# Kernel optimization log

Hardware: AMD Instinct MI355X
Metric: run time of the kernel (lower is better)

Reference implementation:

```python
import jax, jax.numpy as jnp
import numpy as np

PIANO_SAMPLES = 2_621_440          # multiple of 256 (~119 s @ 22050 Hz)
BLOCK = 512
HOP = 256
N_STEPS = PIANO_SAMPLES // HOP      # 10240 loop iterations
N_FRAMES = PIANO_SAMPLES // HOP + 2 # 10242
UPSAMPLE = 256 // 32                # 8, as in F.upsample(scale_factor=8)


def _hamming(n=BLOCK):
    # torch.hamming_window default: periodic=True
    return (0.54 - 0.46 * jnp.cos(2.0 * jnp.pi * jnp.arange(n, dtype=jnp.float32) / n)).astype(jnp.float32)


def _upsample_linear(v, scale):
    # F.upsample(mode='linear', align_corners=False) on a 1D signal
    n = v.shape[0]
    coords = (jnp.arange(n * scale, dtype=jnp.float32) + 0.5) / scale - 0.5
    coords = jnp.clip(coords, 0.0, n - 1.0)
    lo = jnp.floor(coords).astype(jnp.int32)
    hi = jnp.minimum(lo + 1, n - 1)
    w = coords - lo.astype(jnp.float32)
    return v[lo] * (1.0 - w) + v[hi] * w


def setup_inputs() -> dict:
    key = jax.random.key(0)
    k1, k2, k3, k4, k5, k6 = jax.random.split(key, 6)
    return {
        "x": jnp.zeros((1,), jnp.float32),  # unused by the original forward
        "excitation_env": jax.random.uniform(k1, (N_FRAMES * 32,), jnp.float32) * 0.01,
        "tf_real": jax.random.uniform(k2, (N_FRAMES, 257), jnp.float32) * 0.2,
        "tf_imag": jax.random.uniform(k3, (N_FRAMES, 257), jnp.float32) * 0.2,
        "etf_real": jax.random.uniform(k4, (257,), jnp.float32) * 0.2,
        "etf_imag": jax.random.uniform(k5, (257,), jnp.float32) * 0.2,
        # per-step uniform(-1,1) noise (torch draws this inside forward)
        "noise": jax.random.uniform(k6, (N_STEPS, BLOCK), jnp.float32) * 2.0 - 1.0,
    }


def reference(x, excitation_env, tf_real, tf_imag, etf_real, etf_imag, noise):
    tf = (tf_real + 1j * tf_imag).astype(jnp.complex64)      # [N_FRAMES, 257]
    etf = (etf_real + 1j * etf_imag).astype(jnp.complex64)   # [257]
    win = _hamming()

    # excitation envelope: square then linear-upsample x8 -> len PIANO_SAMPLES + 512
    exc = _upsample_linear(excitation_env ** 2, UPSAMPLE)

    # gather all 512-sample excitation windows at hop 256 -> [N_STEPS, 512]
    idx = jnp.arange(N_STEPS)[:, None] * HOP + jnp.arange(BLOCK)[None, :]
    exc_blocks = exc[idx]

    # batched excitation filtering (independent per step -> fully vectorized)
    imp = noise * exc_blocks
    imp = jnp.fft.irfft(jnp.fft.rfft(imp, norm='ortho') * etf, norm='ortho').astype(jnp.float32)

    # impulse added to the *previous* block at steps 1..N_STEPS-1; last block gets none
    imp_next = jnp.concatenate([imp[1:], jnp.zeros((1, BLOCK), imp.dtype)], axis=0)

    def step(s, inp):
        tf_i, inext = inp
        b = win * jnp.fft.irfft(jnp.fft.rfft(s, norm='ortho') * tf_i, norm='ortho').astype(jnp.float32)
        s_next = b + inext
        return s_next, s_next

    s0 = imp[0]  # learned_impulse=False -> first block is the filtered excitation
    _, ys = jax.lax.scan(step, s0, (tf[:N_STEPS], imp_next))

    blocks = jnp.concatenate([s0[None, :], ys], axis=0)  # [N_STEPS+1, 512]

    # overlap-add with hop 256
    n_b = blocks.shape[0]
    out = jnp.zeros((n_b * HOP + (BLOCK - HOP),), blocks.dtype)
    oa_idx = jnp.arange(n_b)[:, None] * HOP + jnp.arange(BLOCK)[None, :]
    out = out.at[oa_idx].add(blocks)
    return out[:PIANO_SAMPLES]
```

## Files before the change

kernel.cpp:

```cpp
#include <hip/hip_runtime.h>
#include <math.h>

#define N_STEPS 10240
#define ROWF2 264
#define ROWF  (ROWF2*2)
#define ENV_N 327744
#define LCH 16

typedef float f4a __attribute__((ext_vector_type(4), aligned(4)));

__device__ inline float2 mkf2(float x, float y) { return make_float2(x, y); }

template<int DIR>
__device__ inline void waveFFT256(float2 v[4], const int l,
                                  const float Tc, const float Ts,
                                  const float ux, const float uy) {
  const int rb = (int)(__brev((unsigned)l) >> 26);
  #pragma unroll
  for (int r = 0; r < 4; ++r) {
    v[r].x = __shfl(v[r].x, rb);
    v[r].y = __shfl(v[r].y, rb);
  }
  #pragma unroll
  for (int s = 0; s < 6; ++s) {
    const int half = 1 << s;
    float wx, wy;
    if (s == 0) { wx = (l & 1) ? -1.f : 1.f; wy = 0.f; }
    else {
      const int idx = (l << (5 - s)) & 63;
      wx = __shfl(Tc, idx);
      float tsv = __shfl(Ts, idx);
      wy = (DIR < 0) ? tsv : -tsv;
    }
    #pragma unroll
    for (int r = 0; r < 4; ++r) {
      float tx = __shfl_xor(v[r].x, half);
      float ty = __shfl_xor(v[r].y, half);
      const bool low = (l & half) == 0;
      float ax = low ? v[r].x : tx, ay = low ? v[r].y : ty;
      float bx = low ? tx : v[r].x, by = low ? ty : v[r].y;
      v[r].x = ax + (wx * bx - wy * by);
      v[r].y = ay + (wx * by + wy * bx);
    }
  }
  const float u2x = ux * ux - uy * uy, u2y = 2.f * ux * uy;
  const float u3x = u2x * ux - u2y * uy, u3y = u2x * uy + u2y * ux;
  float2 t0 = v[0];
  float2 t1 = mkf2(v[1].x * ux - v[1].y * uy, v[1].x * uy + v[1].y * ux);
  float2 t2 = mkf2(v[2].x * u2x - v[2].y * u2y, v[2].x * u2y + v[2].y * u2x);
  float2 t3 = mkf2(v[3].x * u3x - v[3].y * u3y, v[3].x * u3y + v[3].y * u3x);
  float2 p02 = mkf2(t0.x + t2.x, t0.y + t2.y), m02 = mkf2(t0.x - t2.x, t0.y - t2.y);
  float2 p13 = mkf2(t1.x + t3.x, t1.y + t3.y), m13 = mkf2(t1.x - t3.x, t1.y - t3.y);
  v[0] = mkf2(p02.x + p13.x, p02.y + p13.y);
  v[2] = mkf2(p02.x - p13.x, p02.y - p13.y);
  if (DIR < 0) {
    v[1] = mkf2(m02.x + m13.y, m02.y - m13.x);
    v[3] = mkf2(m02.x - m13.y, m02.y + m13.x);
  } else {
    v[1] = mkf2(m02.x - m13.y, m02.y + m13.x);
    v[3] = mkf2(m02.x + m13.y, m02.y - m13.x);
  }
}

__global__ __launch_bounds__(256) void kernA(const float* __restrict__ env,
                                             const float* __restrict__ noise,
                                             const float* __restrict__ tf_re,
                                             const float* __restrict__ etf_re,
                                             const float* __restrict__ etf_im,
                                             float* __restrict__ IMP,
                                             float* __restrict__ T256,
                                             float* __restrict__ I256) {
  const int l = threadIdx.x & 63;
  const int j = blockIdx.x * 4 + (threadIdx.x >> 6);
  float* rowf = IMP + (size_t)j * ROWF;
  float2* row = (float2*)rowf;
  if (j >= N_STEPS) {
    if (j == N_STEPS) {
      #pragma unroll
      for (int r = 0; r < 4; ++r) row[64 * r + l] = mkf2(0.f, 0.f);
      if (l == 0) { row[256] = mkf2(0.f, 0.f); I256[N_STEPS] = 0.f; }
    }
    return;
  }
  const int K = 32 * j + l;
  float e0 = env[K];                e0 *= e0;
  float em = env[max(K - 1, 0)];    em *= em;
  float ep = env[min(K + 1, ENV_N - 1)]; ep *= ep;
  float sm[8];
  #pragma unroll
  for (int u = 0; u < 8; ++u) {
    float val;
    if (u < 4) {
      float fr = 0.5625f + 0.125f * (float)u;
      val = em * (1.f - fr) + e0 * fr;
      if (K == 0) val = e0;
    } else {
      float fr = 0.0625f + 0.125f * (float)(u - 4);
      val = e0 * (1.f - fr) + ep * fr;
    }
    sm[u] = val;
  }
  const float4* np = (const float4*)(noise + (size_t)j * 512 + 8 * l);
  float4 n0 = np[0], n1 = np[1];
  float nn[8] = {n0.x, n0.y, n0.z, n0.w, n1.x, n1.y, n1.z, n1.w};
  float2 v[4];
  #pragma unroll
  for (int r = 0; r < 4; ++r)
    v[r] = mkf2(nn[2 * r] * sm[2 * r], nn[2 * r + 1] * sm[2 * r + 1]);

  float ca, sa; sincosf(-0.01227184630308513f * (float)l, &sa, &ca);
  const float ux = ca * ca - sa * sa, uy = 2.f * ca * sa;
  float Tc, Ts; sincosf(-0.09817477042468103f * (float)l, &Ts, &Tc);

  waveFFT256<-1>(v, l, Tc, Ts, ux, uy);

  float2 Zc[4];
  const int pidx = (64 - l) & 63;
  #pragma unroll
  for (int r = 0; r < 4; ++r) {
    Zc[r].x = __shfl(v[3 - r].x, pidx);
    Zc[r].y = __shfl(v[3 - r].y, pidx);
  }
  float2 z0lane = v[0];
  if (l == 0) { Zc[0] = v[0]; Zc[1] = v[3]; Zc[2] = v[2]; Zc[3] = v[1]; }
  constexpr float crA[4] = {1.f, 0.7071067811865476f, 0.f, -0.7071067811865476f};
  constexpr float srA[4] = {0.f, -0.7071067811865476f, -1.f, -0.7071067811865476f};
  const float FS = 0.04419417382415922f;
  #pragma unroll
  for (int r = 0; r < 4; ++r) {
    float Ex = 0.5f * (v[r].x + Zc[r].x), Ey = 0.5f * (v[r].y - Zc[r].y);
    float Dx = v[r].x - Zc[r].x,          Dy = v[r].y + Zc[r].y;
    float Ox = 0.5f * Dy, Oy = -0.5f * Dx;
    float c  = crA[r] * ca - srA[r] * sa;
    float sn = crA[r] * sa + srA[r] * ca;
    float Wx = (Ex + (c * Ox - sn * Oy)) * FS;
    float Wy = (Ey + (c * Oy + sn * Ox)) * FS;
    int k = 64 * r + l;
    float er = etf_re[k], ei = etf_im[k];
    float Px = Wx * er - Wy * ei;
    float Py = Wx * ei + Wy * er;
    if (k == 0) Py = 0.f;
    row[k] = mkf2(Px, Py);
  }
  if (l == 0) {
    float W256 = (z0lane.x - z0lane.y) * FS;
    float imp256 = W256 * etf_re[256];
    row[256] = mkf2(imp256, 0.f);
    I256[j] = imp256;
    T256[j] = tf_re[(size_t)j * 257 + 256];
  }
}

struct StepBuf { f4a tr, ti; float4 ia, ib; };

__device__ inline void loadStep(StepBuf& b, int i, int l,
                                const float* __restrict__ tf_re,
                                const float* __restrict__ tf_im,
                                const float* __restrict__ IMP) {
  const size_t tb = (size_t)i * 257 + 4 * l;
  b.tr = *(const f4a*)(tf_re + tb);
  b.ti = *(const f4a*)(tf_im + tb);
  const float4* r4 = (const float4*)(IMP + (size_t)(i + 1) * ROWF);
  b.ia = r4[2 * l];
  b.ib = r4[2 * l + 1];
}

__device__ inline void doStep(const StepBuf& b, int l, float tfr256, float imp256,
                              float2& s0, float2& s1, float2& s2, float2& s3,
                              float& s256) {
  float2 y0, y1, y2, y3;
  y0.x = s0.x * b.tr[0] - s0.y * b.ti[0];  y0.y = s0.x * b.ti[0] + s0.y * b.tr[0];
  y1.x = s1.x * b.tr[1] - s1.y * b.ti[1];  y1.y = s1.x * b.ti[1] + s1.y * b.tr[1];
  y2.x = s2.x * b.tr[2] - s2.y * b.ti[2];  y2.y = s2.x * b.ti[2] + s2.y * b.tr[2];
  y3.x = s3.x * b.tr[3] - s3.y * b.ti[3];  y3.y = s3.x * b.ti[3] + s3.y * b.tr[3];
  if (l == 0) y0.y = 0.f;
  float Y256 = tfr256 * s256;
  float phx = __shfl_up(y3.x, 1), phy = __shfl_up(y3.y, 1);
  float nlx = __shfl_down(y0.x, 1), nly = __shfl_down(y0.y, 1);
  float2 p0 = (l == 0)  ? mkf2(y1.x, -y1.y) : mkf2(phx, phy);
  float2 n3 = (l == 63) ? mkf2(Y256, 0.f)   : mkf2(nlx, nly);
  float y255x = __shfl(y3.x, 63);
  const float A = 0.54f, Bc = 0.23f;
  float2 c0, c1, c2, c3;
  c0.x = A * y0.x - Bc * (p0.x + y1.x);  c0.y = A * y0.y - Bc * (p0.y + y1.y);
  c1.x = A * y1.x - Bc * (y0.x + y2.x);  c1.y = A * y1.y - Bc * (y0.y + y2.y);
  c2.x = A * y2.x - Bc * (y1.x + y3.x);  c2.y = A * y2.y - Bc * (y1.y + y3.y);
  c3.x = A * y3.x - Bc * (y2.x + n3.x);  c3.y = A * y3.y - Bc * (y2.y + n3.y);
  float C256 = A * Y256 - 0.46f * y255x;
  s0.x = c0.x + b.ia.x;  s0.y = c0.y + b.ia.y;
  s1.x = c1.x + b.ia.z;  s1.y = c1.y + b.ia.w;
  s2.x = c2.x + b.ib.x;  s2.y = c2.y + b.ib.y;
  s3.x = c3.x + b.ib.z;  s3.y = c3.y + b.ib.w;
  s256 = C256 + imp256;
}

__global__ __launch_bounds__(256, 2) void kernBC(const float* __restrict__ tf_re,
                                                 const float* __restrict__ tf_im,
                                                 const float* __restrict__ IMP,
                                                 const float* __restrict__ T256,
                                                 const float* __restrict__ I256,
                                                 float* __restrict__ out) {
  const int c = blockIdx.x, tid = threadIdx.x;
  const int l = tid & 63, w = tid >> 6;
  const int j0 = c * LCH;
  const int w0 = (c > 0) ? (j0 - 9) : 0;
  const int lastStep = (c > 0) ? (j0 + 14) : 15;

  __shared__ float2 ybuf[17][256];

  float t256v = T256[min(w0 + l, N_STEPS - 1)];
  float i256v = I256[min(w0 + 1 + l, N_STEPS)];

  float2 s0 = mkf2(0.f, 0.f), s1 = s0, s2 = s0, s3 = s0;
  float s256 = 0.f;
  float2 rs[5][4];
  float rn[5];
  #pragma unroll
  for (int q = 0; q < 5; ++q) {
    rs[q][0] = rs[q][1] = rs[q][2] = rs[q][3] = mkf2(0.f, 0.f);
    rn[q] = 0.f;
  }

  if (c == 0) {
    const float4* r4 = (const float4*)IMP;
    float4 a = r4[2 * l], bb = r4[2 * l + 1];
    s0 = mkf2(a.x, a.y);  s1 = mkf2(a.z, a.w);
    s2 = mkf2(bb.x, bb.y); s3 = mkf2(bb.z, bb.w);
    s256 = IMP[512];
    if (w == 1) { rs[0][0]=s0; rs[0][1]=s1; rs[0][2]=s2; rs[0][3]=s3; rn[0]=s256; }
  }

  StepBuf b0, b1, b2, b3;
  loadStep(b0, w0 + 0, l, tf_re, tf_im, IMP);
  loadStep(b1, w0 + 1, l, tf_re, tf_im, IMP);
  loadStep(b2, w0 + 2, l, tf_re, tf_im, IMP);
  loadStep(b3, w0 + 3, l, tf_re, tf_im, IMP);

  #define SAVEIF(KK) \
    if ((KK) >= 0 && (KK) <= 16 && (((KK) & 3) == w)) { \
      const int _q = (((KK) > 0 ? (KK) : 0)) >> 2; \
      rs[_q][0]=s0; rs[_q][1]=s1; rs[_q][2]=s2; rs[_q][3]=s3; rn[_q]=s256; }

  #define STEP(BUF, M, KK) { \
    const float tfr_ = __shfl(t256v, (M)); \
    const float im2_ = __shfl(i256v, (M)); \
    doStep(BUF, l, tfr_, im2_, s0, s1, s2, s3, s256); \
    SAVEIF(KK) \
    { int nx = w0 + (M) + 4; nx = (nx > lastStep) ? lastStep : nx; \
      loadStep(BUF, nx, l, tf_re, tf_im, IMP); } }

  if (c > 0) {
    STEP(b0,0,-7)  STEP(b1,1,-6)  STEP(b2,2,-5)  STEP(b3,3,-4)
    STEP(b0,4,-3)  STEP(b1,5,-2)  STEP(b2,6,-1)  STEP(b3,7,0)
    STEP(b0,8,1)   STEP(b1,9,2)   STEP(b2,10,3)  STEP(b3,11,4)
    STEP(b0,12,5)  STEP(b1,13,6)  STEP(b2,14,7)  STEP(b3,15,8)
    STEP(b0,16,9)  STEP(b1,17,10) STEP(b2,18,11) STEP(b3,19,12)
    STEP(b0,20,13) STEP(b1,21,14) STEP(b2,22,15) STEP(b3,23,16)
  } else {
    STEP(b0,0,2)   STEP(b1,1,3)   STEP(b2,2,4)   STEP(b3,3,5)
    STEP(b0,4,6)   STEP(b1,5,7)   STEP(b2,6,8)   STEP(b3,7,9)
    STEP(b0,8,10)  STEP(b1,9,11)  STEP(b2,10,12) STEP(b3,11,13)
    STEP(b0,12,14) STEP(b1,13,15) STEP(b2,14,16) STEP(b3,15,17)
  }
  #undef STEP
  #undef SAVEIF

  float cu, su; sincosf(0.02454369260617026f * (float)l, &su, &cu);
  const float clC = cu * cu - su * su, slC = 2.f * cu * su;
  float Tc, Ts; sincosf(-0.09817477042468103f * (float)l, &Ts, &Tc);
  constexpr float crC[4] = {1.f, 0.9999247018391445f, 0.9996988186962042f, 0.9993223845883495f};
  constexpr float srC[4] = {0.f, 0.0122715382857199f, 0.0245412285229123f, 0.0368072229413588f};
  const float ISC = 0.08838834764831845f;
  const int pidx = (64 - l) & 63;

  #pragma unroll
  for (int q = 0; q < 5; ++q) {
    const int k = 4 * q + w;
    if (k <= 16) {
      float2 W0 = rs[q][0], W1 = rs[q][1], W2 = rs[q][2], W3 = rs[q][3];
      float w256 = rn[q];
      float2 W[4] = {W0, W1, W2, W3};
      float2 Wm[4];
      Wm[0].x = __shfl(W0.x, pidx);
      Wm[0].y = __shfl(W0.y, pidx);
      if (l == 0) Wm[0] = mkf2(w256, 0.f);
      Wm[1].x = __shfl_xor(W3.x, 63);  Wm[1].y = __shfl_xor(W3.y, 63);
      Wm[2].x = __shfl_xor(W2.x, 63);  Wm[2].y = __shfl_xor(W2.y, 63);
      Wm[3].x = __shfl_xor(W1.x, 63);  Wm[3].y = __shfl_xor(W1.y, 63);
      float2 v[4];
      #pragma unroll
      for (int rr = 0; rr < 4; ++rr) {
        float Ex = 0.5f * (W[rr].x + Wm[rr].x), Ey = 0.5f * (W[rr].y - Wm[rr].y);
        float Dx = W[rr].x - Wm[rr].x,          Dy = W[rr].y + Wm[rr].y;
        float cc  = clC * crC[rr] - slC * srC[rr];
        float sn  = clC * srC[rr] + slC * crC[rr];
        float Ox = 0.5f * (cc * Dx - sn * Dy);
        float Oy = 0.5f * (cc * Dy + sn * Dx);
        v[rr] = mkf2(Ex - Oy, Ey + Ox);
      }
      waveFFT256<+1>(v, l, Tc, Ts, cu, su);
      #pragma unroll
      for (int rr = 0; rr < 4; ++rr)
        ybuf[k][64 * rr + l] = mkf2(v[rr].x * ISC, v[rr].y * ISC);
    }
  }

  __syncthreads();

  float2* out2 = (float2*)out;
  const size_t base = (size_t)j0 * 128;
  for (int idx = tid; idx < 2048; idx += 256) {
    const int k = idx >> 7, t2 = idx & 127;
    float2 a = ybuf[k + 1][t2];
    float2 p = ybuf[k][128 + t2];
    out2[base + idx] = mkf2(a.x + p.x, a.y + p.y);
  }
}

extern "C" void kernel_launch(void* const* d_in, const int* in_sizes, int n_in,
                              void* d_out, int out_size, void* d_ws, size_t ws_size,
                              hipStream_t stream) {
  const float* env    = (const float*)d_in[1];
  const float* tf_re  = (const float*)d_in[2];
  const float* tf_im  = (const float*)d_in[3];
  const float* etf_re = (const float*)d_in[4];
  const float* etf_im = (const float*)d_in[5];
  const float* noise  = (const float*)d_in[6];
  float* out = (float*)d_out;

  float* wsf = (float*)d_ws;
  float* IMP  = wsf;
  float* T256 = wsf + (size_t)(N_STEPS + 1) * ROWF;
  float* I256 = T256 + N_STEPS;

  kernA<<<(N_STEPS / 4) + 1, 256, 0, stream>>>(env, noise, tf_re, etf_re, etf_im,
                                               IMP, T256, I256);
  kernBC<<<N_STEPS / LCH, 256, 0, stream>>>(tf_re, tf_im, IMP, T256, I256, out);
}
```

Before: 49.73 us.

## Fuse excitation filtering into recurrence kernel via shared-memory impulse rows

```diff
diff --git a/kernel.cpp b/kernel.cpp
--- a/kernel.cpp
+++ b/kernel.cpp
@@ -2,8 +2,6 @@
 #include <math.h>
 
 #define N_STEPS 10240
-#define ROWF2 264
-#define ROWF  (ROWF2*2)
 #define ENV_N 327744
 #define LCH 16
 
@@ -62,26 +60,13 @@
   }
 }
 
-__global__ __launch_bounds__(256) void kernA(const float* __restrict__ env,
-                                             const float* __restrict__ noise,
-                                             const float* __restrict__ tf_re,
-                                             const float* __restrict__ etf_re,
-                                             const float* __restrict__ etf_im,
-                                             float* __restrict__ IMP,
-                                             float* __restrict__ T256,
-                                             float* __restrict__ I256) {
-  const int l = threadIdx.x & 63;
-  const int j = blockIdx.x * 4 + (threadIdx.x >> 6);
-  float* rowf = IMP + (size_t)j * ROWF;
-  float2* row = (float2*)rowf;
-  if (j >= N_STEPS) {
-    if (j == N_STEPS) {
-      #pragma unroll
-      for (int r = 0; r < 4; ++r) row[64 * r + l] = mkf2(0.f, 0.f);
-      if (l == 0) { row[256] = mkf2(0.f, 0.f); I256[N_STEPS] = 0.f; }
-    }
-    return;
-  }
+__device__ inline void impRow(int j, int l, float2* __restrict__ row,
+                              const float* __restrict__ env,
+                              const float* __restrict__ noise,
+                              const float* __restrict__ etf_re,
+                              const float* __restrict__ etf_im,
+                              float ca, float sa, float ux, float uy,
+                              float Tc, float Ts) {
   const int K = 32 * j + l;
   float e0 = env[K];                e0 *= e0;
   float em = env[max(K - 1, 0)];    em *= em;
@@ -107,10 +92,6 @@
   #pragma unroll
   for (int r = 0; r < 4; ++r)
     v[r] = mkf2(nn[2 * r] * sm[2 * r], nn[2 * r + 1] * sm[2 * r + 1]);
-
-  float ca, sa; sincosf(-0.01227184630308513f * (float)l, &sa, &ca);
-  const float ux = ca * ca - sa * sa, uy = 2.f * ca * sa;
-  float Tc, Ts; sincosf(-0.09817477042468103f * (float)l, &Ts, &Tc);
 
   waveFFT256<-1>(v, l, Tc, Ts, ux, uy);
 
@@ -144,28 +125,22 @@
   }
   if (l == 0) {
     float W256 = (z0lane.x - z0lane.y) * FS;
-    float imp256 = W256 * etf_re[256];
-    row[256] = mkf2(imp256, 0.f);
-    I256[j] = imp256;
-    T256[j] = tf_re[(size_t)j * 257 + 256];
-  }
-}
-
-struct StepBuf { f4a tr, ti; float4 ia, ib; };
-
-__device__ inline void loadStep(StepBuf& b, int i, int l,
-                                const float* __restrict__ tf_re,
-                                const float* __restrict__ tf_im,
-                                const float* __restrict__ IMP) {
+    row[256] = mkf2(W256 * etf_re[256], 0.f);
+  }
+}
+
+struct StepBuf { f4a tr, ti; };
+
+__device__ inline void loadTF(StepBuf& b, int i, int l,
+                              const float* __restrict__ tf_re,
+                              const float* __restrict__ tf_im) {
   const size_t tb = (size_t)i * 257 + 4 * l;
   b.tr = *(const f4a*)(tf_re + tb);
   b.ti = *(const f4a*)(tf_im + tb);
-  const float4* r4 = (const float4*)(IMP + (size_t)(i + 1) * ROWF);
-  b.ia = r4[2 * l];
-  b.ib = r4[2 * l + 1];
-}
-
-__device__ inline void doStep(const StepBuf& b, int l, float tfr256, float imp256,
+}
+
+__device__ inline void doStep(const StepBuf& b, const float4& ia, const float4& ib,
+                              int l, float tfr256, float imp256,
                               float2& s0, float2& s1, float2& s2, float2& s3,
                               float& s256) {
   float2 y0, y1, y2, y3;
@@ -187,29 +162,50 @@
   c2.x = A * y2.x - Bc * (y1.x + y3.x);  c2.y = A * y2.y - Bc * (y1.y + y3.y);
   c3.x = A * y3.x - Bc * (y2.x + n3.x);  c3.y = A * y3.y - Bc * (y2.y + n3.y);
   float C256 = A * Y256 - 0.46f * y255x;
-  s0.x = c0.x + b.ia.x;  s0.y = c0.y + b.ia.y;
-  s1.x = c1.x + b.ia.z;  s1.y = c1.y + b.ia.w;
-  s2.x = c2.x + b.ib.x;  s2.y = c2.y + b.ib.y;
-  s3.x = c3.x + b.ib.z;  s3.y = c3.y + b.ib.w;
+  s0.x = c0.x + ia.x;  s0.y = c0.y + ia.y;
+  s1.x = c1.x + ia.z;  s1.y = c1.y + ia.w;
+  s2.x = c2.x + ib.x;  s2.y = c2.y + ib.y;
+  s3.x = c3.x + ib.z;  s3.y = c3.y + ib.w;
   s256 = C256 + imp256;
 }
 
-__global__ __launch_bounds__(256, 2) void kernBC(const float* __restrict__ tf_re,
-                                                 const float* __restrict__ tf_im,
-                                                 const float* __restrict__ IMP,
-                                                 const float* __restrict__ T256,
-                                                 const float* __restrict__ I256,
-                                                 float* __restrict__ out) {
+__global__ __launch_bounds__(256, 2) void kernABC(const float* __restrict__ env,
+                                                  const float* __restrict__ noise,
+                                                  const float* __restrict__ tf_re,
+                                                  const float* __restrict__ tf_im,
+                                                  const float* __restrict__ etf_re,
+                                                  const float* __restrict__ etf_im,
+                                                  float* __restrict__ out) {
   const int c = blockIdx.x, tid = threadIdx.x;
   const int l = tid & 63, w = tid >> 6;
   const int j0 = c * LCH;
   const int w0 = (c > 0) ? (j0 - 9) : 0;
   const int lastStep = (c > 0) ? (j0 + 14) : 15;
-
-  __shared__ float2 ybuf[17][256];
-
-  float t256v = T256[min(w0 + l, N_STEPS - 1)];
-  float i256v = I256[min(w0 + 1 + l, N_STEPS)];
+  const int NR = (c > 0) ? 24 : 17;
+  const int rowbase = (c > 0) ? (j0 - 8) : 0;
+  const int IMPOFF = (c > 0) ? 0 : 1;
+
+  __shared__ float2 SH[24 * 258];
+
+  float t256v = tf_re[(size_t)min(w0 + l, N_STEPS - 1) * 257 + 256];
+  StepBuf b0, b1, b2, b3;
+  loadTF(b0, w0 + 0, l, tf_re, tf_im);
+  loadTF(b1, w0 + 1, l, tf_re, tf_im);
+  loadTF(b2, w0 + 2, l, tf_re, tf_im);
+  loadTF(b3, w0 + 3, l, tf_re, tf_im);
+
+  float ca, sa; sincosf(-0.01227184630308513f * (float)l, &sa, &ca);
+  const float ux = ca * ca - sa * sa, uy = 2.f * ca * sa;
+  float Tc, Ts; sincosf(-0.09817477042468103f * (float)l, &Ts, &Tc);
+  float cu, su; sincosf(0.02454369260617026f * (float)l, &su, &cu);
+  const float clC = cu * cu - su * su, slC = 2.f * cu * su;
+
+  for (int t = w; t < NR; t += 4)
+    impRow(rowbase + t, l, SH + t * 258, env, noise, etf_re, etf_im,
+           ca, sa, ux, uy, Tc, Ts);
+  __syncthreads();
+
+  const float i256v = SH[(size_t)min(l + IMPOFF, NR - 1) * 258 + 256].x;
 
   float2 s0 = mkf2(0.f, 0.f), s1 = s0, s2 = s0, s3 = s0;
   float s256 = 0.f;
@@ -222,19 +218,13 @@
   }
 
   if (c == 0) {
-    const float4* r4 = (const float4*)IMP;
+    const float4* r4 = (const float4*)SH;
     float4 a = r4[2 * l], bb = r4[2 * l + 1];
     s0 = mkf2(a.x, a.y);  s1 = mkf2(a.z, a.w);
     s2 = mkf2(bb.x, bb.y); s3 = mkf2(bb.z, bb.w);
-    s256 = IMP[512];
+    s256 = SH[256].x;
     if (w == 1) { rs[0][0]=s0; rs[0][1]=s1; rs[0][2]=s2; rs[0][3]=s3; rn[0]=s256; }
   }
-
-  StepBuf b0, b1, b2, b3;
-  loadStep(b0, w0 + 0, l, tf_re, tf_im, IMP);
-  loadStep(b1, w0 + 1, l, tf_re, tf_im, IMP);
-  loadStep(b2, w0 + 2, l, tf_re, tf_im, IMP);
-  loadStep(b3, w0 + 3, l, tf_re, tf_im, IMP);
 
   #define SAVEIF(KK) \
     if ((KK) >= 0 && (KK) <= 16 && (((KK) & 3) == w)) { \
@@ -244,10 +234,13 @@
   #define STEP(BUF, M, KK) { \
     const float tfr_ = __shfl(t256v, (M)); \
     const float im2_ = __shfl(i256v, (M)); \
-    doStep(BUF, l, tfr_, im2_, s0, s1, s2, s3, s256); \
+    const float4* ims = (const float4*)(SH + ((M) + IMPOFF) * 258); \
+    const float4 ia = ims[2 * l]; \
+    const float4 ib = ims[2 * l + 1]; \
+    doStep(BUF, ia, ib, l, tfr_, im2_, s0, s1, s2, s3, s256); \
     SAVEIF(KK) \
     { int nx = w0 + (M) + 4; nx = (nx > lastStep) ? lastStep : nx; \
-      loadStep(BUF, nx, l, tf_re, tf_im, IMP); } }
+      loadTF(BUF, nx, l, tf_re, tf_im); } }
 
   if (c > 0) {
     STEP(b0,0,-7)  STEP(b1,1,-6)  STEP(b2,2,-5)  STEP(b3,3,-4)
@@ -265,9 +258,9 @@
   #undef STEP
   #undef SAVEIF
 
-  float cu, su; sincosf(0.02454369260617026f * (float)l, &su, &cu);
-  const float clC = cu * cu - su * su, slC = 2.f * cu * su;
-  float Tc, Ts; sincosf(-0.09817477042468103f * (float)l, &Ts, &Tc);
+  __syncthreads();
+
+  float2 (*ybuf)[256] = (float2(*)[256])SH;
   constexpr float crC[4] = {1.f, 0.9999247018391445f, 0.9996988186962042f, 0.9993223845883495f};
   constexpr float srC[4] = {0.f, 0.0122715382857199f, 0.0245412285229123f, 0.0368072229413588f};
   const float ISC = 0.08838834764831845f;
@@ -328,12 +321,6 @@
   const float* noise  = (const float*)d_in[6];
   float* out = (float*)d_out;
 
-  float* wsf = (float*)d_ws;
-  float* IMP  = wsf;
-  float* T256 = wsf + (size_t)(N_STEPS + 1) * ROWF;
-  float* I256 = T256 + N_STEPS;
-
-  kernA<<<(N_STEPS / 4) + 1, 256, 0, stream>>>(env, noise, tf_re, etf_re, etf_im,
-                                               IMP, T256, I256);
-  kernBC<<<N_STEPS / LCH, 256, 0, stream>>>(tf_re, tf_im, IMP, T256, I256, out);
-}
+  kernABC<<<N_STEPS / LCH, 256, 0, stream>>>(env, noise, tf_re, tf_im,
+                                             etf_re, etf_im, out);
+}
```

After: 55.81 us. 12.2% more time.

## Double chunk length per block, deepen prefetch, stash saved states in LDS

Applied to the files above, without the earlier changes.

```diff
diff --git a/kernel.cpp b/kernel.cpp
--- a/kernel.cpp
+++ b/kernel.cpp
@@ -5,7 +5,7 @@
 #define ROWF2 264
 #define ROWF  (ROWF2*2)
 #define ENV_N 327744
-#define LCH 16
+#define LCH 32
 
 typedef float f4a __attribute__((ext_vector_type(4), aligned(4)));
 
@@ -204,22 +204,15 @@
   const int l = tid & 63, w = tid >> 6;
   const int j0 = c * LCH;
   const int w0 = (c > 0) ? (j0 - 9) : 0;
-  const int lastStep = (c > 0) ? (j0 + 14) : 15;
-
-  __shared__ float2 ybuf[17][256];
+  const int lastStep = (c > 0) ? (j0 + 30) : 31;
+
+  __shared__ __align__(16) float2 SH[33 * 258];
 
   float t256v = T256[min(w0 + l, N_STEPS - 1)];
   float i256v = I256[min(w0 + 1 + l, N_STEPS)];
 
   float2 s0 = mkf2(0.f, 0.f), s1 = s0, s2 = s0, s3 = s0;
   float s256 = 0.f;
-  float2 rs[5][4];
-  float rn[5];
-  #pragma unroll
-  for (int q = 0; q < 5; ++q) {
-    rs[q][0] = rs[q][1] = rs[q][2] = rs[q][3] = mkf2(0.f, 0.f);
-    rn[q] = 0.f;
-  }
 
   if (c == 0) {
     const float4* r4 = (const float4*)IMP;
@@ -227,40 +220,59 @@
     s0 = mkf2(a.x, a.y);  s1 = mkf2(a.z, a.w);
     s2 = mkf2(bb.x, bb.y); s3 = mkf2(bb.z, bb.w);
     s256 = IMP[512];
-    if (w == 1) { rs[0][0]=s0; rs[0][1]=s1; rs[0][2]=s2; rs[0][3]=s3; rn[0]=s256; }
-  }
-
-  StepBuf b0, b1, b2, b3;
+    if (w == 1) {
+      float4* d4 = (float4*)(SH + 1 * 258);
+      d4[2 * l]     = make_float4(s0.x, s0.y, s1.x, s1.y);
+      d4[2 * l + 1] = make_float4(s2.x, s2.y, s3.x, s3.y);
+      if (l == 0) SH[1 * 258 + 256] = mkf2(s256, 0.f);
+    }
+  }
+
+  StepBuf b0, b1, b2, b3, b4, b5, b6, b7;
   loadStep(b0, w0 + 0, l, tf_re, tf_im, IMP);
   loadStep(b1, w0 + 1, l, tf_re, tf_im, IMP);
   loadStep(b2, w0 + 2, l, tf_re, tf_im, IMP);
   loadStep(b3, w0 + 3, l, tf_re, tf_im, IMP);
+  loadStep(b4, w0 + 4, l, tf_re, tf_im, IMP);
+  loadStep(b5, w0 + 5, l, tf_re, tf_im, IMP);
+  loadStep(b6, w0 + 6, l, tf_re, tf_im, IMP);
+  loadStep(b7, w0 + 7, l, tf_re, tf_im, IMP);
 
   #define SAVEIF(KK) \
-    if ((KK) >= 0 && (KK) <= 16 && (((KK) & 3) == w)) { \
-      const int _q = (((KK) > 0 ? (KK) : 0)) >> 2; \
-      rs[_q][0]=s0; rs[_q][1]=s1; rs[_q][2]=s2; rs[_q][3]=s3; rn[_q]=s256; }
+    if ((KK) >= 0 && (KK) <= 32 && (((KK) & 3) == w)) { \
+      float4* d4 = (float4*)(SH + (KK) * 258); \
+      d4[2 * l]     = make_float4(s0.x, s0.y, s1.x, s1.y); \
+      d4[2 * l + 1] = make_float4(s2.x, s2.y, s3.x, s3.y); \
+      if (l == 0) SH[(KK) * 258 + 256] = mkf2(s256, 0.f); }
 
   #define STEP(BUF, M, KK) { \
     const float tfr_ = __shfl(t256v, (M)); \
     const float im2_ = __shfl(i256v, (M)); \
     doStep(BUF, l, tfr_, im2_, s0, s1, s2, s3, s256); \
     SAVEIF(KK) \
-    { int nx = w0 + (M) + 4; nx = (nx > lastStep) ? lastStep : nx; \
+    { int nx = w0 + (M) + 8; nx = (nx > lastStep) ? lastStep : nx; \
       loadStep(BUF, nx, l, tf_re, tf_im, IMP); } }
 
   if (c > 0) {
-    STEP(b0,0,-7)  STEP(b1,1,-6)  STEP(b2,2,-5)  STEP(b3,3,-4)
-    STEP(b0,4,-3)  STEP(b1,5,-2)  STEP(b2,6,-1)  STEP(b3,7,0)
-    STEP(b0,8,1)   STEP(b1,9,2)   STEP(b2,10,3)  STEP(b3,11,4)
-    STEP(b0,12,5)  STEP(b1,13,6)  STEP(b2,14,7)  STEP(b3,15,8)
-    STEP(b0,16,9)  STEP(b1,17,10) STEP(b2,18,11) STEP(b3,19,12)
-    STEP(b0,20,13) STEP(b1,21,14) STEP(b2,22,15) STEP(b3,23,16)
+    STEP(b0,0,-7)   STEP(b1,1,-6)   STEP(b2,2,-5)   STEP(b3,3,-4)
+    STEP(b4,4,-3)   STEP(b5,5,-2)   STEP(b6,6,-1)   STEP(b7,7,0)
+    STEP(b0,8,1)    STEP(b1,9,2)    STEP(b2,10,3)   STEP(b3,11,4)
+    STEP(b4,12,5)   STEP(b5,13,6)   STEP(b6,14,7)   STEP(b7,15,8)
+    STEP(b0,16,9)   STEP(b1,17,10)  STEP(b2,18,11)  STEP(b3,19,12)
+    STEP(b4,20,13)  STEP(b5,21,14)  STEP(b6,22,15)  STEP(b7,23,16)
+    STEP(b0,24,17)  STEP(b1,25,18)  STEP(b2,26,19)  STEP(b3,27,20)
+    STEP(b4,28,21)  STEP(b5,29,22)  STEP(b6,30,23)  STEP(b7,31,24)
+    STEP(b0,32,25)  STEP(b1,33,26)  STEP(b2,34,27)  STEP(b3,35,28)
+    STEP(b4,36,29)  STEP(b5,37,30)  STEP(b6,38,31)  STEP(b7,39,32)
   } else {
-    STEP(b0,0,2)   STEP(b1,1,3)   STEP(b2,2,4)   STEP(b3,3,5)
-    STEP(b0,4,6)   STEP(b1,5,7)   STEP(b2,6,8)   STEP(b3,7,9)
-    STEP(b0,8,10)  STEP(b1,9,11)  STEP(b2,10,12) STEP(b3,11,13)
-    STEP(b0,12,14) STEP(b1,13,15) STEP(b2,14,16) STEP(b3,15,17)
+    STEP(b0,0,2)    STEP(b1,1,3)    STEP(b2,2,4)    STEP(b3,3,5)
+    STEP(b4,4,6)    STEP(b5,5,7)    STEP(b6,6,8)    STEP(b7,7,9)
+    STEP(b0,8,10)   STEP(b1,9,11)   STEP(b2,10,12)  STEP(b3,11,13)
+    STEP(b4,12,14)  STEP(b5,13,15)  STEP(b6,14,16)  STEP(b7,15,17)
+    STEP(b0,16,18)  STEP(b1,17,19)  STEP(b2,18,20)  STEP(b3,19,21)
+    STEP(b4,20,22)  STEP(b5,21,23)  STEP(b6,22,24)  STEP(b7,23,25)
+    STEP(b0,24,26)  STEP(b1,25,27)  STEP(b2,26,28)  STEP(b3,27,29)
+    STEP(b4,28,30)  STEP(b5,29,31)  STEP(b6,30,32)  STEP(b7,31,33)
   }
   #undef STEP
   #undef SAVEIF
@@ -274,34 +286,41 @@
   const int pidx = (64 - l) & 63;
 
   #pragma unroll
-  for (int q = 0; q < 5; ++q) {
+  for (int q = 0; q < 9; ++q) {
     const int k = 4 * q + w;
-    if (k <= 16) {
-      float2 W0 = rs[q][0], W1 = rs[q][1], W2 = rs[q][2], W3 = rs[q][3];
-      float w256 = rn[q];
-      float2 W[4] = {W0, W1, W2, W3};
-      float2 Wm[4];
-      Wm[0].x = __shfl(W0.x, pidx);
-      Wm[0].y = __shfl(W0.y, pidx);
-      if (l == 0) Wm[0] = mkf2(w256, 0.f);
-      Wm[1].x = __shfl_xor(W3.x, 63);  Wm[1].y = __shfl_xor(W3.y, 63);
-      Wm[2].x = __shfl_xor(W2.x, 63);  Wm[2].y = __shfl_xor(W2.y, 63);
-      Wm[3].x = __shfl_xor(W1.x, 63);  Wm[3].y = __shfl_xor(W1.y, 63);
-      float2 v[4];
-      #pragma unroll
-      for (int rr = 0; rr < 4; ++rr) {
-        float Ex = 0.5f * (W[rr].x + Wm[rr].x), Ey = 0.5f * (W[rr].y - Wm[rr].y);
-        float Dx = W[rr].x - Wm[rr].x,          Dy = W[rr].y + Wm[rr].y;
-        float cc  = clC * crC[rr] - slC * srC[rr];
-        float sn  = clC * srC[rr] + slC * crC[rr];
-        float Ox = 0.5f * (cc * Dx - sn * Dy);
-        float Oy = 0.5f * (cc * Dy + sn * Dx);
-        v[rr] = mkf2(Ex - Oy, Ey + Ox);
+    if (k <= 32) {
+      float2* rowp = SH + k * 258;
+      if (c == 0 && k == 0) {
+        #pragma unroll
+        for (int rr = 0; rr < 4; ++rr) rowp[64 * rr + l] = mkf2(0.f, 0.f);
+      } else {
+        const float4* r4 = (const float4*)rowp;
+        float4 a = r4[2 * l], bb = r4[2 * l + 1];
+        float2 W[4] = {mkf2(a.x, a.y), mkf2(a.z, a.w), mkf2(bb.x, bb.y), mkf2(bb.z, bb.w)};
+        float w256 = rowp[256].x;
+        float2 Wm[4];
+        Wm[0].x = __shfl(W[0].x, pidx);
+        Wm[0].y = __shfl(W[0].y, pidx);
+        if (l == 0) Wm[0] = mkf2(w256, 0.f);
+        Wm[1].x = __shfl_xor(W[3].x, 63);  Wm[1].y = __shfl_xor(W[3].y, 63);
+        Wm[2].x = __shfl_xor(W[2].x, 63);  Wm[2].y = __shfl_xor(W[2].y, 63);
+        Wm[3].x = __shfl_xor(W[1].x, 63);  Wm[3].y = __shfl_xor(W[1].y, 63);
+        float2 v[4];
+        #pragma unroll
+        for (int rr = 0; rr < 4; ++rr) {
+          float Ex = 0.5f * (W[rr].x + Wm[rr].x), Ey = 0.5f * (W[rr].y - Wm[rr].y);
+          float Dx = W[rr].x - Wm[rr].x,          Dy = W[rr].y + Wm[rr].y;
+          float cc  = clC * crC[rr] - slC * srC[rr];
+          float sn  = clC * srC[rr] + slC * crC[rr];
+          float Ox = 0.5f * (cc * Dx - sn * Dy);
+          float Oy = 0.5f * (cc * Dy + sn * Dx);
+          v[rr] = mkf2(Ex - Oy, Ey + Ox);
+        }
+        waveFFT256<+1>(v, l, Tc, Ts, cu, su);
+        #pragma unroll
+        for (int rr = 0; rr < 4; ++rr)
+          rowp[64 * rr + l] = mkf2(v[rr].x * ISC, v[rr].y * ISC);
       }
-      waveFFT256<+1>(v, l, Tc, Ts, cu, su);
-      #pragma unroll
-      for (int rr = 0; rr < 4; ++rr)
-        ybuf[k][64 * rr + l] = mkf2(v[rr].x * ISC, v[rr].y * ISC);
     }
   }
 
@@ -309,10 +328,10 @@
 
   float2* out2 = (float2*)out;
   const size_t base = (size_t)j0 * 128;
-  for (int idx = tid; idx < 2048; idx += 256) {
+  for (int idx = tid; idx < 4096; idx += 256) {
     const int k = idx >> 7, t2 = idx & 127;
-    float2 a = ybuf[k + 1][t2];
-    float2 p = ybuf[k][128 + t2];
+    float2 a = SH[(k + 1) * 258 + t2];
+    float2 p = SH[k * 258 + 128 + t2];
     out2[base + idx] = mkf2(a.x + p.x, a.y + p.y);
   }
 }
```

Result: slower. 61.23 us (+23.1%).
